# Kernel optimization log

Measured on AMD Instinct MI355X. Metric: run time of the kernel, lower is better.

## Reference

```python
import jax, jax.numpy as jnp
import numpy as np

B, N, C_IN, C_OUT, BASIS = 8, 128, 64, 64, 15
AVG_NOBJ = 49.0
NEG_SLOPE = 0.01  # torch LeakyReLU default


def eops_2_to_2_sum(x, average_nobj=AVG_NOBJ):
    """x: [B, C, N, N] -> [B, C, 15, N, N].
    5 order-zero ops + 10 sum-aggregation ops (sums normalized by average_nobj,
    double sums by average_nobj**2, as in PELICAN's 'sum' aggregation)."""
    n = x.shape[-1]
    eye = jnp.eye(n, dtype=x.dtype)                       # [N, N]
    d = jnp.diagonal(x, axis1=-2, axis2=-1)               # [B, C, N]
    rowsum = x.sum(-1) / average_nobj                      # [B, C, N]
    colsum = x.sum(-2) / average_nobj                      # [B, C, N]
    trace = d.sum(-1) / average_nobj                       # [B, C]
    allsum = x.sum((-2, -1)) / (average_nobj ** 2)         # [B, C]
    bc = lambda v: jnp.broadcast_to(v, x.shape)
    ops = [
        # --- order zero (no aggregation) ---
        d[..., :, None] * eye,                 # diag(A) embedded on diagonal
        bc(d[..., :, None]),                   # A_ii broadcast along j
        bc(d[..., None, :]),                   # A_jj broadcast along i
        x,                                     # identity
        jnp.swapaxes(x, -1, -2),               # transpose
        # --- aggregation ops ---
        rowsum[..., :, None] * eye,            # row sums on diagonal
        colsum[..., :, None] * eye,            # col sums on diagonal
        trace[..., None, None] * eye,          # trace on diagonal
        allsum[..., None, None] * eye,         # total sum on diagonal
        bc(rowsum[..., :, None]),              # rowsum_i broadcast along j
        bc(rowsum[..., None, :]),              # rowsum_j broadcast along i
        bc(colsum[..., :, None]),              # colsum_i broadcast along j
        bc(colsum[..., None, :]),              # colsum_j broadcast along i
        bc(trace[..., None, None]),            # trace broadcast everywhere
        bc(allsum[..., None, None]),           # total sum broadcast everywhere
    ]
    return jnp.stack(ops, axis=2)              # [B, C, 15, N, N]


def setup_inputs() -> dict:
    key = jax.random.key(0)
    ks = jax.random.split(key, 5)
    inputs = jax.random.normal(ks[0], (B, N, N, C_IN), jnp.float32)
    mask = jnp.ones((B, N, N, 1), jnp.float32)
    nobj = jnp.full((B,), float(N), jnp.float32)
    s_b = float(np.sqrt(1.0 / BASIS))
    s_d = float(np.sqrt(1.0 / C_IN))
    coefs00 = jax.random.normal(ks[1], (C_IN, BASIS), jnp.float32) * s_b
    coefs01 = jax.random.normal(ks[2], (C_OUT, BASIS), jnp.float32) * s_b
    coefs10 = jax.random.normal(ks[3], (C_IN, C_OUT), jnp.float32) * s_d
    coefs11 = jax.random.normal(ks[4], (C_IN, C_OUT), jnp.float32) * s_d
    bias = jnp.zeros((C_OUT,), jnp.float32)
    diag_bias = jnp.zeros((C_OUT,), jnp.float32)
    return {"inputs": inputs, "mask": mask, "nobj": nobj,
            "coefs00": coefs00, "coefs01": coefs01,
            "coefs10": coefs10, "coefs11": coefs11,
            "bias": bias, "diag_bias": diag_bias}


def reference(inputs, mask, nobj, coefs00, coefs01, coefs10, coefs11, bias, diag_bias):
    # inputs: [B, N, N, C_in] -> channels-first for basis construction
    x = jnp.transpose(inputs, (0, 3, 1, 2))                     # [B, C, N, N]
    ops = eops_2_to_2_sum(x)                                    # [B, C, 15, N, N]
    # low-rank reconstructed coefficient tensor [C_in, C_out, 15]
    coefs = (coefs00[:, None, :] * coefs10[:, :, None]
             + coefs01[None, :, :] * coefs11[:, :, None])
    out = jnp.einsum('dsb,ndbij->nijs', coefs, ops)             # [B, N, N, C_out]
    eye = jnp.eye(inputs.shape[1], dtype=out.dtype)[None, :, :, None]
    out = out + bias[None, None, None, :] + eye * diag_bias[None, None, None, :]
    out = jax.nn.leaky_relu(out, NEG_SLOPE)
    return out * mask
```

## Files before the change

### kernel.cpp

```cpp
#include <hip/hip_runtime.h>

#define BB 8
#define NN 128
#define CC 64
#define NT 16
static constexpr float INV_A = 1.0f / 49.0f;

#define OFF_C    0
#define OFF_CB   61440
#define OFF_RS   65536
#define OFF_CS   131072
#define OFF_DV   196608
#define OFF_U1   263168
#define OFF_U2   328704
#define OFF_DG   394240
#define OFF_XB   459776

typedef __attribute__((ext_vector_type(8))) short v8s;
typedef __attribute__((ext_vector_type(4))) float v4f;

static __device__ inline unsigned pack2bf(float a, float b) {
    union { float f; unsigned u; } ua, ub; ua.f = a; ub.f = b;
    return ((ua.u + 0x8000u) >> 16) | ((ub.u + 0x8000u) & 0xffff0000u);
}
static __device__ inline unsigned short f2bf(float a) {
    union { float f; unsigned u; } ua; ua.f = a;
    return (unsigned short)((ua.u + 0x8000u) >> 16);
}

__global__ void k_pre(const float* __restrict__ in,
                      const float* __restrict__ c00, const float* __restrict__ c01,
                      const float* __restrict__ c10, const float* __restrict__ c11,
                      float* __restrict__ ws) {
    if (blockIdx.x >= 512) {
        int idx = (blockIdx.x - 512) * 256 + threadIdx.x;
        if (idx < 15 * 4096) {
            int b = idx >> 12; int r = idx & 4095; int d = r >> 6; int s = r & 63;
            ws[OFF_C + idx] = c00[d * 15 + b] * c10[d * 64 + s] + c01[s * 15 + b] * c11[d * 64 + s];
        } else if (idx < 15 * 4096 + 8192) {
            int k = idx - 15 * 4096;
            int which = k >> 12;
            int r = k & 4095; int s = r >> 6; int d = r & 63;
            int b = 3 + which;
            float v = c00[d * 15 + b] * c10[d * 64 + s] + c01[s * 15 + b] * c11[d * 64 + s];
            unsigned short* cb = (unsigned short*)(ws + OFF_CB);
            cb[s * 128 + which * 64 + d] = f2bf(v);
        }
        return;
    }
    __shared__ float4 part[4][4][16];
    int mode = blockIdx.x >> 8;
    int bb = blockIdx.x & 255;
    int n = bb >> 5; int g0 = (bb & 31) * 4;
    int t = threadIdx.x;
    int q = t >> 6; int ii = (t >> 4) & 3; int d4 = t & 15;
    float4 acc = make_float4(0.f, 0.f, 0.f, 0.f);
    if (mode == 0) {
        int i = g0 + ii;
        float4 dvv = acc; bool hd = false;
        const float* base = in + ((size_t)(n * NN + i)) * NN * CC + d4 * 4;
        unsigned short* xB = (unsigned short*)(ws + OFF_XB)
                           + ((size_t)(n * NN + i)) * NN * CC + d4 * 4;
        for (int j = q * 32; j < q * 32 + 32; ++j) {
            float4 v = *(const float4*)(base + (size_t)j * CC);
            acc.x += v.x; acc.y += v.y; acc.z += v.z; acc.w += v.w;
            uint2 pk; pk.x = pack2bf(v.x, v.y); pk.y = pack2bf(v.z, v.w);
            *(uint2*)(xB + (size_t)j * CC) = pk;
            if (j == i) { dvv = v; hd = true; }
        }
        if (hd) *(float4*)(ws + OFF_DV + ((size_t)(n * NN + i)) * CC + d4 * 4) = dvv;
    } else {
        int j = g0 + ii;
        for (int i = q * 32; i < q * 32 + 32; ++i) {
            float4 v = *(const float4*)(in + (((size_t)(n * NN + i)) * NN + j) * CC + d4 * 4);
            acc.x += v.x; acc.y += v.y; acc.z += v.z; acc.w += v.w;
        }
    }
    part[q][ii][d4] = acc;
    __syncthreads();
    if (t < 64) {
        int i2 = t >> 4; int dd = t & 15;
        float4 a = part[0][i2][dd], b = part[1][i2][dd], c = part[2][i2][dd], d = part[3][i2][dd];
        float4 s;
        s.x = (a.x + b.x + c.x + d.x) * INV_A;
        s.y = (a.y + b.y + c.y + d.y) * INV_A;
        s.z = (a.z + b.z + c.z + d.z) * INV_A;
        s.w = (a.w + b.w + c.w + d.w) * INV_A;
        *(float4*)(ws + (mode ? OFF_CS : OFF_RS) + ((size_t)(n * NN + g0 + i2)) * CC + dd * 4) = s;
    }
}

__global__ __launch_bounds__(256, 4) void k_uv(const float* __restrict__ bias,
                                               const float* __restrict__ dbias,
                                               float* __restrict__ ws) {
    __shared__ float trL[64], asL[64];
    __shared__ float pU1[4][4][64], pU2[4][4][64], pDG[4][4][64];
    __shared__ float pS[4][64], pDGc[4][64];
    int n = blockIdx.x >> 5; int i0 = (blockIdx.x & 31) * 4;
    int t = threadIdx.x;
    int s = t & 63; int q = t >> 6;

    {
        float tr = 0.f, as = 0.f;
        #pragma unroll 4
        for (int e = 0; e < 32; ++e) {
            int i = q * 32 + e;
            tr += ws[OFF_DV + ((size_t)(n * NN + i)) * CC + s];
            as += ws[OFF_RS + ((size_t)(n * NN + i)) * CC + s];
        }
        pS[q][s] = tr; pDGc[q][s] = as;
        __syncthreads();
        if (t < 64) {
            trL[t] = (pS[0][t] + pS[1][t] + pS[2][t] + pS[3][t]) * INV_A;
            asL[t] = (pDGc[0][t] + pDGc[1][t] + pDGc[2][t] + pDGc[3][t]) * INV_A;
        }
        __syncthreads();
    }

    const float* C = ws + OFF_C;
    float aU1[4] = {0, 0, 0, 0}, aU2[4] = {0, 0, 0, 0}, aDG[4] = {0, 0, 0, 0};
    float aS = 0.f, aDGc = 0.f;
    #pragma unroll
    for (int c4 = 0; c4 < 4; ++c4) {
        int dc = q * 4 + c4;
        float tr4[4], as4[4], dv4[4][4], rs4[4][4], cs4[4][4];
        #pragma unroll
        for (int k = 0; k < 4; ++k) { tr4[k] = trL[dc * 4 + k]; as4[k] = asL[dc * 4 + k]; }
        #pragma unroll
        for (int ii = 0; ii < 4; ++ii) {
            size_t ro = ((size_t)(n * NN + i0 + ii)) * CC + dc * 4;
            float4 v = *(const float4*)(ws + OFF_DV + ro);
            dv4[ii][0] = v.x; dv4[ii][1] = v.y; dv4[ii][2] = v.z; dv4[ii][3] = v.w;
            float4 r = *(const float4*)(ws + OFF_RS + ro);
            rs4[ii][0] = r.x; rs4[ii][1] = r.y; rs4[ii][2] = r.z; rs4[ii][3] = r.w;
            float4 c = *(const float4*)(ws + OFF_CS + ro);
            cs4[ii][0] = c.x; cs4[ii][1] = c.y; cs4[ii][2] = c.z; cs4[ii][3] = c.w;
        }
        #pragma unroll
        for (int k = 0; k < 4; ++k) {
            int d = dc * 4 + k;
            const float* Cd = C + d * 64 + s;
            float c0 = Cd[0 * 4096], c1 = Cd[1 * 4096], c2 = Cd[2 * 4096];
            float c5 = Cd[5 * 4096], c6 = Cd[6 * 4096], c7 = Cd[7 * 4096];
            float c8 = Cd[8 * 4096], c9 = Cd[9 * 4096], c10v = Cd[10 * 4096];
            float c11v = Cd[11 * 4096], c12v = Cd[12 * 4096];
            float c13 = Cd[13 * 4096], c14 = Cd[14 * 4096];
            aS += c13 * tr4[k] + c14 * as4[k];
            aDGc += c7 * tr4[k] + c8 * as4[k];
            #pragma unroll
            for (int ii = 0; ii < 4; ++ii) {
                aU1[ii] += c1 * dv4[ii][k] + c9 * rs4[ii][k] + c11v * cs4[ii][k];
                aU2[ii] += c2 * dv4[ii][k] + c10v * rs4[ii][k] + c12v * cs4[ii][k];
                aDG[ii] += c0 * dv4[ii][k] + c5 * rs4[ii][k] + c6 * cs4[ii][k];
            }
        }
    }
    #pragma unroll
    for (int ii = 0; ii < 4; ++ii) {
        pU1[q][ii][s] = aU1[ii]; pU2[q][ii][s] = aU2[ii]; pDG[q][ii][s] = aDG[ii];
    }
    pS[q][s] = aS; pDGc[q][s] = aDGc;
    __syncthreads();

    int fi = q;
    float u1 = pU1[0][fi][s] + pU1[1][fi][s] + pU1[2][fi][s] + pU1[3][fi][s];
    float u2 = pU2[0][fi][s] + pU2[1][fi][s] + pU2[2][fi][s] + pU2[3][fi][s];
    float dg = pDG[0][fi][s] + pDG[1][fi][s] + pDG[2][fi][s] + pDG[3][fi][s];
    float aSt = pS[0][s] + pS[1][s] + pS[2][s] + pS[3][s];
    float aDGct = pDGc[0][s] + pDGc[1][s] + pDGc[2][s] + pDGc[3][s];
    size_t row = ((size_t)(n * NN + i0 + fi)) * CC + s;
    ws[OFF_U1 + row] = u1 + aSt + bias[s];
    ws[OFF_U2 + row] = u2;
    ws[OFF_DG + row] = dg + aDGct + dbias[s];
}

__global__ __launch_bounds__(256, 4) void k_main(
        const float* __restrict__ mask,
        const float* __restrict__ ws, float* __restrict__ out) {
    __shared__ __align__(16) unsigned char smem[34816];
    unsigned short* Ab = (unsigned short*)smem;
    unsigned short* Bb = (unsigned short*)(smem + 17408);
    float* Obuf = (float*)smem;

    int blk = blockIdx.x;
    int n = blk / 136; int rem = blk - n * 136;
    int I = 0;
    { int rr = rem; while (rr >= NT - I) { rr -= NT - I; ++I; } rem = rr; }
    int J = I + rem;
    int i0 = I * 8, j0 = J * 8;
    int t = threadIdx.x;
    int tp = t >> 4; int c = t & 15;

    const unsigned short* cb = (const unsigned short*)(ws + OFF_CB);
    #pragma unroll
    for (int e = 0; e < 4; ++e) {
        int s = e * 16 + tp;
        float4 v = *(const float4*)(cb + s * 128 + c * 8);
        *(float4*)((unsigned char*)(Bb + s * 136 + c * 8)) = v;
    }
    const unsigned short* xb = (const unsigned short*)(ws + OFF_XB);
    #pragma unroll
    for (int e = 0; e < 4; ++e) {
        int idx = e * 256 + t;
        int chunk = idx & 7; int row = idx >> 3;
        int hh = row >> 6; int p = row & 63;
        int ii = p >> 3, jj = p & 7;
        int gi = hh ? (j0 + jj) : (i0 + ii);
        int gj = hh ? (i0 + ii) : (j0 + jj);
        float4 v = *(const float4*)(xb + (((size_t)(n * NN + gi)) * NN + gj) * CC + chunk * 8);
        *(float4*)((unsigned char*)(Ab + p * 136 + hh * 64 + chunk * 8)) = v;
    }
    __syncthreads();

    int w = t >> 6; int l = t & 63;
    int r16 = l & 15; int quad = l >> 4;
    int arow = w * 16 + r16;
    v8s af[4];
    #pragma unroll
    for (int kk = 0; kk < 4; ++kk)
        af[kk] = *(const v8s*)(Ab + arow * 136 + kk * 32 + quad * 8);
    v4f acc1[4], acc2[4];
    #pragma unroll
    for (int st = 0; st < 4; ++st) { acc1[st] = 0.f; acc2[st] = 0.f; }
    #pragma unroll
    for (int kk = 0; kk < 4; ++kk) {
        #pragma unroll
        for (int st = 0; st < 4; ++st) {
            v8s bfr = *(const v8s*)(Bb + (st * 16 + r16) * 136 + kk * 32 + quad * 8);
            acc1[st] = __builtin_amdgcn_mfma_f32_16x16x32_bf16(af[kk], bfr, acc1[st], 0, 0, 0);
            acc2[st] = __builtin_amdgcn_mfma_f32_16x16x32_bf16(af[(kk + 2) & 3], bfr, acc2[st], 0, 0, 0);
        }
    }

    #pragma unroll
    for (int st = 0; st < 4; ++st)
        #pragma unroll
        for (int reg = 0; reg < 4; ++reg)
            Obuf[(w * 16 + quad * 4 + reg) * 68 + st * 16 + r16] = acc1[st][reg];
    __syncthreads();
    #pragma unroll
    for (int e = 0; e < 4; ++e) {
        int p = e * 16 + tp;
        int gi = i0 + (p >> 3), gj = j0 + (p & 7);
        size_t prow = ((size_t)(n * NN + gi));
        float4 v = *(const float4*)(Obuf + p * 68 + c * 4);
        float4 u1 = *(const float4*)(ws + OFF_U1 + prow * CC + c * 4);
        float4 u2 = *(const float4*)(ws + OFF_U2 + ((size_t)(n * NN + gj)) * CC + c * 4);
        v.x += u1.x + u2.x; v.y += u1.y + u2.y; v.z += u1.z + u2.z; v.w += u1.w + u2.w;
        if (gi == gj) {
            float4 dg = *(const float4*)(ws + OFF_DG + prow * CC + c * 4);
            v.x += dg.x; v.y += dg.y; v.z += dg.z; v.w += dg.w;
        }
        v.x = v.x > 0.f ? v.x : 0.01f * v.x;
        v.y = v.y > 0.f ? v.y : 0.01f * v.y;
        v.z = v.z > 0.f ? v.z : 0.01f * v.z;
        v.w = v.w > 0.f ? v.w : 0.01f * v.w;
        float m = mask[prow * NN + gj];
        v.x *= m; v.y *= m; v.z *= m; v.w *= m;
        *(float4*)(out + (prow * NN + gj) * CC + c * 4) = v;
    }

    if (I == J) return;
    __syncthreads();
    #pragma unroll
    for (int st = 0; st < 4; ++st)
        #pragma unroll
        for (int reg = 0; reg < 4; ++reg)
            Obuf[(w * 16 + quad * 4 + reg) * 68 + st * 16 + r16] = acc2[st][reg];
    __syncthreads();
    #pragma unroll
    for (int e = 0; e < 4; ++e) {
        int p = e * 16 + tp;
        int gi = j0 + (p & 7), gj = i0 + (p >> 3);
        size_t prow = ((size_t)(n * NN + gi));
        float4 v = *(const float4*)(Obuf + p * 68 + c * 4);
        float4 u1 = *(const float4*)(ws + OFF_U1 + prow * CC + c * 4);
        float4 u2 = *(const float4*)(ws + OFF_U2 + ((size_t)(n * NN + gj)) * CC + c * 4);
        v.x += u1.x + u2.x; v.y += u1.y + u2.y; v.z += u1.z + u2.z; v.w += u1.w + u2.w;
        v.x = v.x > 0.f ? v.x : 0.01f * v.x;
        v.y = v.y > 0.f ? v.y : 0.01f * v.y;
        v.z = v.z > 0.f ? v.z : 0.01f * v.z;
        v.w = v.w > 0.f ? v.w : 0.01f * v.w;
        float m = mask[prow * NN + gj];
        v.x *= m; v.y *= m; v.z *= m; v.w *= m;
        *(float4*)(out + (prow * NN + gj) * CC + c * 4) = v;
    }
}

extern "C" void kernel_launch(void* const* d_in, const int* in_sizes, int n_in,
                              void* d_out, int out_size, void* d_ws, size_t ws_size,
                              hipStream_t stream) {
    const float* inputs = (const float*)d_in[0];
    const float* mask   = (const float*)d_in[1];
    const float* c00 = (const float*)d_in[3];
    const float* c01 = (const float*)d_in[4];
    const float* c10 = (const float*)d_in[5];
    const float* c11 = (const float*)d_in[6];
    const float* bias  = (const float*)d_in[7];
    const float* dbias = (const float*)d_in[8];
    float* out = (float*)d_out;
    float* ws = (float*)d_ws;

    k_pre <<<784, 256, 0, stream>>>(inputs, c00, c01, c10, c11, ws);
    k_uv  <<<256, 256, 0, stream>>>(bias, dbias, ws);
    k_main<<<8 * 136, 256, 0, stream>>>(mask, ws, out);
}
```

Measured before the change: 139.0 us.

## Fuse k_uv into k_main, computing row/col vectors via bf16 MFMA per tile

Drops the separate k_uv kernel. Each k_main block now stages bf16 copies of the DV/RS/CS rows it needs into shared memory and computes the U1/U2 row/column terms with extra MFMA calls against bf16 coefficient slices that k_pre prepares. The trace and allsum reductions and the diagonal term are recomputed per block. This saves one kernel launch and the global round trip for U1/U2/DG, at the cost of redundant per-block work (every block reduces all 128 rows for the trace), lower bf16 precision for the U terms, and more shared memory with occupancy dropped to 3.

```diff
diff --git a/kernel.cpp b/kernel.cpp
--- a/kernel.cpp
+++ b/kernel.cpp
@@ -8,13 +8,12 @@
 
 #define OFF_C    0
 #define OFF_CB   61440
-#define OFF_RS   65536
-#define OFF_CS   131072
-#define OFF_DV   196608
-#define OFF_U1   263168
-#define OFF_U2   328704
-#define OFF_DG   394240
-#define OFF_XB   459776
+#define OFF_CU1  65536
+#define OFF_CU2  71680
+#define OFF_RS   77824
+#define OFF_CS   143360
+#define OFF_DV   208896
+#define OFF_XB   274432
 
 typedef __attribute__((ext_vector_type(8))) short v8s;
 typedef __attribute__((ext_vector_type(4))) float v4f;
@@ -26,6 +25,9 @@
 static __device__ inline unsigned short f2bf(float a) {
     union { float f; unsigned u; } ua; ua.f = a;
     return (unsigned short)((ua.u + 0x8000u) >> 16);
+}
+static __device__ inline float bf2f(unsigned short h) {
+    union { unsigned u; float f; } c; c.u = ((unsigned)h) << 16; return c.f;
 }
 
 __global__ void k_pre(const float* __restrict__ in,
@@ -34,17 +36,28 @@
                       float* __restrict__ ws) {
     if (blockIdx.x >= 512) {
         int idx = (blockIdx.x - 512) * 256 + threadIdx.x;
-        if (idx < 15 * 4096) {
+        if (idx < 61440) {
             int b = idx >> 12; int r = idx & 4095; int d = r >> 6; int s = r & 63;
             ws[OFF_C + idx] = c00[d * 15 + b] * c10[d * 64 + s] + c01[s * 15 + b] * c11[d * 64 + s];
-        } else if (idx < 15 * 4096 + 8192) {
-            int k = idx - 15 * 4096;
+        } else if (idx < 69632) {
+            int k = idx - 61440;
             int which = k >> 12;
             int r = k & 4095; int s = r >> 6; int d = r & 63;
             int b = 3 + which;
             float v = c00[d * 15 + b] * c10[d * 64 + s] + c01[s * 15 + b] * c11[d * 64 + s];
             unsigned short* cb = (unsigned short*)(ws + OFF_CB);
             cb[s * 128 + which * 64 + d] = f2bf(v);
+        } else {
+            int e = idx - 69632;
+            int which = e >= 12288;
+            int r = which ? e - 12288 : e;
+            int s = r / 192; int k = r - s * 192;
+            int f = k >> 6; int d = k & 63;
+            const int b1[3] = {1, 9, 11}, b2[3] = {2, 10, 12};
+            int b = which ? b2[f] : b1[f];
+            float v = c00[d * 15 + b] * c10[d * 64 + s] + c01[s * 15 + b] * c11[d * 64 + s];
+            unsigned short* cu = (unsigned short*)(ws + (which ? OFF_CU2 : OFF_CU1));
+            cu[s * 192 + k] = f2bf(v);
         }
         return;
     }
@@ -90,97 +103,21 @@
     }
 }
 
-__global__ __launch_bounds__(256, 4) void k_uv(const float* __restrict__ bias,
-                                               const float* __restrict__ dbias,
-                                               float* __restrict__ ws) {
-    __shared__ float trL[64], asL[64];
-    __shared__ float pU1[4][4][64], pU2[4][4][64], pDG[4][4][64];
-    __shared__ float pS[4][64], pDGc[4][64];
-    int n = blockIdx.x >> 5; int i0 = (blockIdx.x & 31) * 4;
-    int t = threadIdx.x;
-    int s = t & 63; int q = t >> 6;
-
-    {
-        float tr = 0.f, as = 0.f;
-        #pragma unroll 4
-        for (int e = 0; e < 32; ++e) {
-            int i = q * 32 + e;
-            tr += ws[OFF_DV + ((size_t)(n * NN + i)) * CC + s];
-            as += ws[OFF_RS + ((size_t)(n * NN + i)) * CC + s];
-        }
-        pS[q][s] = tr; pDGc[q][s] = as;
-        __syncthreads();
-        if (t < 64) {
-            trL[t] = (pS[0][t] + pS[1][t] + pS[2][t] + pS[3][t]) * INV_A;
-            asL[t] = (pDGc[0][t] + pDGc[1][t] + pDGc[2][t] + pDGc[3][t]) * INV_A;
-        }
-        __syncthreads();
-    }
-
-    const float* C = ws + OFF_C;
-    float aU1[4] = {0, 0, 0, 0}, aU2[4] = {0, 0, 0, 0}, aDG[4] = {0, 0, 0, 0};
-    float aS = 0.f, aDGc = 0.f;
-    #pragma unroll
-    for (int c4 = 0; c4 < 4; ++c4) {
-        int dc = q * 4 + c4;
-        float tr4[4], as4[4], dv4[4][4], rs4[4][4], cs4[4][4];
-        #pragma unroll
-        for (int k = 0; k < 4; ++k) { tr4[k] = trL[dc * 4 + k]; as4[k] = asL[dc * 4 + k]; }
-        #pragma unroll
-        for (int ii = 0; ii < 4; ++ii) {
-            size_t ro = ((size_t)(n * NN + i0 + ii)) * CC + dc * 4;
-            float4 v = *(const float4*)(ws + OFF_DV + ro);
-            dv4[ii][0] = v.x; dv4[ii][1] = v.y; dv4[ii][2] = v.z; dv4[ii][3] = v.w;
-            float4 r = *(const float4*)(ws + OFF_RS + ro);
-            rs4[ii][0] = r.x; rs4[ii][1] = r.y; rs4[ii][2] = r.z; rs4[ii][3] = r.w;
-            float4 c = *(const float4*)(ws + OFF_CS + ro);
-            cs4[ii][0] = c.x; cs4[ii][1] = c.y; cs4[ii][2] = c.z; cs4[ii][3] = c.w;
-        }
-        #pragma unroll
-        for (int k = 0; k < 4; ++k) {
-            int d = dc * 4 + k;
-            const float* Cd = C + d * 64 + s;
-            float c0 = Cd[0 * 4096], c1 = Cd[1 * 4096], c2 = Cd[2 * 4096];
-            float c5 = Cd[5 * 4096], c6 = Cd[6 * 4096], c7 = Cd[7 * 4096];
-            float c8 = Cd[8 * 4096], c9 = Cd[9 * 4096], c10v = Cd[10 * 4096];
-            float c11v = Cd[11 * 4096], c12v = Cd[12 * 4096];
-            float c13 = Cd[13 * 4096], c14 = Cd[14 * 4096];
-            aS += c13 * tr4[k] + c14 * as4[k];
-            aDGc += c7 * tr4[k] + c8 * as4[k];
-            #pragma unroll
-            for (int ii = 0; ii < 4; ++ii) {
-                aU1[ii] += c1 * dv4[ii][k] + c9 * rs4[ii][k] + c11v * cs4[ii][k];
-                aU2[ii] += c2 * dv4[ii][k] + c10v * rs4[ii][k] + c12v * cs4[ii][k];
-                aDG[ii] += c0 * dv4[ii][k] + c5 * rs4[ii][k] + c6 * cs4[ii][k];
-            }
-        }
-    }
-    #pragma unroll
-    for (int ii = 0; ii < 4; ++ii) {
-        pU1[q][ii][s] = aU1[ii]; pU2[q][ii][s] = aU2[ii]; pDG[q][ii][s] = aDG[ii];
-    }
-    pS[q][s] = aS; pDGc[q][s] = aDGc;
-    __syncthreads();
-
-    int fi = q;
-    float u1 = pU1[0][fi][s] + pU1[1][fi][s] + pU1[2][fi][s] + pU1[3][fi][s];
-    float u2 = pU2[0][fi][s] + pU2[1][fi][s] + pU2[2][fi][s] + pU2[3][fi][s];
-    float dg = pDG[0][fi][s] + pDG[1][fi][s] + pDG[2][fi][s] + pDG[3][fi][s];
-    float aSt = pS[0][s] + pS[1][s] + pS[2][s] + pS[3][s];
-    float aDGct = pDGc[0][s] + pDGc[1][s] + pDGc[2][s] + pDGc[3][s];
-    size_t row = ((size_t)(n * NN + i0 + fi)) * CC + s;
-    ws[OFF_U1 + row] = u1 + aSt + bias[s];
-    ws[OFF_U2 + row] = u2;
-    ws[OFF_DG + row] = dg + aDGct + dbias[s];
-}
-
-__global__ __launch_bounds__(256, 4) void k_main(
-        const float* __restrict__ mask,
+__global__ __launch_bounds__(256, 3) void k_main(
+        const float* __restrict__ mask, const float* __restrict__ bias,
+        const float* __restrict__ dbias,
         const float* __restrict__ ws, float* __restrict__ out) {
-    __shared__ __align__(16) unsigned char smem[34816];
-    unsigned short* Ab = (unsigned short*)smem;
-    unsigned short* Bb = (unsigned short*)(smem + 17408);
+    __shared__ __align__(16) unsigned char smem[52608];
+    unsigned short* Ab  = (unsigned short*)smem;
+    unsigned short* Bb  = (unsigned short*)(smem + 17408);
+    unsigned short* RVb = (unsigned short*)(smem + 34816);
+    float* U1L = (float*)(smem + 41216);
+    float* U2L = (float*)(smem + 45568);
+    float* dgL = (float*)(smem + 49920);
+    float* trL = (float*)(smem + 52096);
+    float* asL = (float*)(smem + 52352);
     float* Obuf = (float*)smem;
+    float* trP  = U1L;
 
     int blk = blockIdx.x;
     int n = blk / 136; int rem = blk - n * 136;
@@ -210,6 +147,42 @@
         float4 v = *(const float4*)(xb + (((size_t)(n * NN + gi)) * NN + gj) * CC + chunk * 8);
         *(float4*)((unsigned char*)(Ab + p * 136 + hh * 64 + chunk * 8)) = v;
     }
+    #pragma unroll
+    for (int r2 = 0; r2 < 2; ++r2) {
+        int ci = t + r2 * 256;
+        if (ci < 384) {
+            int row = ci / 24; int remc = ci - row * 24;
+            int f = remc >> 3; int ch = remc & 7;
+            int grow = row < 8 ? (i0 + row) : (j0 + row - 8);
+            int foff = (f == 0) ? OFF_DV : (f == 1 ? OFF_RS : OFF_CS);
+            const float* src = ws + foff + ((size_t)(n * NN + grow)) * CC + ch * 8;
+            float4 a = *(const float4*)(src);
+            float4 b = *(const float4*)(src + 4);
+            uint4 pk;
+            pk.x = pack2bf(a.x, a.y); pk.y = pack2bf(a.z, a.w);
+            pk.z = pack2bf(b.x, b.y); pk.w = pack2bf(b.z, b.w);
+            *(uint4*)((unsigned char*)(RVb + row * 200 + f * 64 + ch * 8)) = pk;
+        }
+    }
+    int q = t >> 6; int s0 = t & 63;
+    {
+        float pd = 0.f, pr = 0.f;
+        #pragma unroll 4
+        for (int e = 0; e < 32; ++e) {
+            int i = q * 32 + e;
+            pd += ws[OFF_DV + ((size_t)(n * NN + i)) * CC + s0];
+            pr += ws[OFF_RS + ((size_t)(n * NN + i)) * CC + s0];
+        }
+        trP[q * 64 + s0] = pd;
+        trP[(4 + q) * 64 + s0] = pr;
+    }
+    __syncthreads();
+    if (t < 128) {
+        int h = t >> 6; int ss = t & 63;
+        const float* p = trP + h * 256;
+        float v = p[ss] + p[64 + ss] + p[128 + ss] + p[192 + ss];
+        (h ? asL : trL)[ss] = v * INV_A;
+    }
     __syncthreads();
 
     int w = t >> 6; int l = t & 63;
@@ -231,24 +204,87 @@
             acc2[st] = __builtin_amdgcn_mfma_f32_16x16x32_bf16(af[(kk + 2) & 3], bfr, acc2[st], 0, 0, 0);
         }
     }
+    v4f aU1 = 0.f, aU2 = 0.f;
+    {
+        const unsigned short* cu1 = (const unsigned short*)(ws + OFF_CU1);
+        const unsigned short* cu2 = (const unsigned short*)(ws + OFF_CU2);
+        int sg = w * 16 + r16;
+        #pragma unroll
+        for (int kk = 0; kk < 6; ++kk) {
+            v8s a1 = *(const v8s*)(cu1 + sg * 192 + kk * 32 + quad * 8);
+            v8s a2 = *(const v8s*)(cu2 + sg * 192 + kk * 32 + quad * 8);
+            v8s bv = *(const v8s*)(RVb + r16 * 200 + kk * 32 + quad * 8);
+            aU1 = __builtin_amdgcn_mfma_f32_16x16x32_bf16(a1, bv, aU1, 0, 0, 0);
+            aU2 = __builtin_amdgcn_mfma_f32_16x16x32_bf16(a2, bv, aU2, 0, 0, 0);
+        }
+    }
+    float sS[4] = {0.f, 0.f, 0.f, 0.f};
+    {
+        const float* C13 = ws + OFF_C + 13 * 4096;
+        const float* C14 = ws + OFF_C + 14 * 4096;
+        for (int d = 0; d < 64; ++d) {
+            float4 a = *(const float4*)(C13 + d * 64 + c * 4);
+            float4 b = *(const float4*)(C14 + d * 64 + c * 4);
+            float tv = trL[d], av = asL[d];
+            sS[0] += tv * a.x + av * b.x;
+            sS[1] += tv * a.y + av * b.y;
+            sS[2] += tv * a.z + av * b.z;
+            sS[3] += tv * a.w + av * b.w;
+        }
+    }
+    if (I == J) {
+        const float* Cb0 = ws + OFF_C;
+        float dg0 = 0.f, dg1 = 0.f, dgc = 0.f;
+        int rg = t >> 6;
+        for (int d = 0; d < 64; ++d) {
+            float c0v = Cb0[0 * 4096 + d * 64 + s0];
+            float c5v = Cb0[5 * 4096 + d * 64 + s0];
+            float c6v = Cb0[6 * 4096 + d * 64 + s0];
+            float c7v = Cb0[7 * 4096 + d * 64 + s0];
+            float c8v = Cb0[8 * 4096 + d * 64 + s0];
+            float dva = bf2f(RVb[rg * 200 + d]);
+            float rsa = bf2f(RVb[rg * 200 + 64 + d]);
+            float csa = bf2f(RVb[rg * 200 + 128 + d]);
+            float dvb = bf2f(RVb[(rg + 4) * 200 + d]);
+            float rsb = bf2f(RVb[(rg + 4) * 200 + 64 + d]);
+            float csb = bf2f(RVb[(rg + 4) * 200 + 128 + d]);
+            dg0 += c0v * dva + c5v * rsa + c6v * csa;
+            dg1 += c0v * dvb + c5v * rsb + c6v * csb;
+            dgc += c7v * trL[d] + c8v * asL[d];
+        }
+        float db = dbias[s0];
+        dgL[rg * 68 + s0] = dg0 + dgc + db;
+        dgL[(rg + 4) * 68 + s0] = dg1 + dgc + db;
+    }
 
     #pragma unroll
     for (int st = 0; st < 4; ++st)
         #pragma unroll
         for (int reg = 0; reg < 4; ++reg)
             Obuf[(w * 16 + quad * 4 + reg) * 68 + st * 16 + r16] = acc1[st][reg];
-    __syncthreads();
+    #pragma unroll
+    for (int reg = 0; reg < 4; ++reg) {
+        U1L[r16 * 68 + w * 16 + quad * 4 + reg] = aU1[reg];
+        U2L[r16 * 68 + w * 16 + quad * 4 + reg] = aU2[reg];
+    }
+    __syncthreads();
+
+    float4 bias4 = *(const float4*)(bias + c * 4);
     #pragma unroll
     for (int e = 0; e < 4; ++e) {
         int p = e * 16 + tp;
-        int gi = i0 + (p >> 3), gj = j0 + (p & 7);
+        int ii = p >> 3, jj = p & 7;
+        int gi = i0 + ii, gj = j0 + jj;
         size_t prow = ((size_t)(n * NN + gi));
         float4 v = *(const float4*)(Obuf + p * 68 + c * 4);
-        float4 u1 = *(const float4*)(ws + OFF_U1 + prow * CC + c * 4);
-        float4 u2 = *(const float4*)(ws + OFF_U2 + ((size_t)(n * NN + gj)) * CC + c * 4);
-        v.x += u1.x + u2.x; v.y += u1.y + u2.y; v.z += u1.z + u2.z; v.w += u1.w + u2.w;
+        float4 u1 = *(const float4*)(U1L + ii * 68 + c * 4);
+        float4 u2 = *(const float4*)(U2L + (8 + jj) * 68 + c * 4);
+        v.x += u1.x + u2.x + sS[0] + bias4.x;
+        v.y += u1.y + u2.y + sS[1] + bias4.y;
+        v.z += u1.z + u2.z + sS[2] + bias4.z;
+        v.w += u1.w + u2.w + sS[3] + bias4.w;
         if (gi == gj) {
-            float4 dg = *(const float4*)(ws + OFF_DG + prow * CC + c * 4);
+            float4 dg = *(const float4*)(dgL + ii * 68 + c * 4);
             v.x += dg.x; v.y += dg.y; v.z += dg.z; v.w += dg.w;
         }
         v.x = v.x > 0.f ? v.x : 0.01f * v.x;
@@ -271,12 +307,16 @@
     #pragma unroll
     for (int e = 0; e < 4; ++e) {
         int p = e * 16 + tp;
-        int gi = j0 + (p & 7), gj = i0 + (p >> 3);
+        int ii = p >> 3, jj = p & 7;
+        int gi = j0 + jj, gj = i0 + ii;
         size_t prow = ((size_t)(n * NN + gi));
         float4 v = *(const float4*)(Obuf + p * 68 + c * 4);
-        float4 u1 = *(const float4*)(ws + OFF_U1 + prow * CC + c * 4);
-        float4 u2 = *(const float4*)(ws + OFF_U2 + ((size_t)(n * NN + gj)) * CC + c * 4);
-        v.x += u1.x + u2.x; v.y += u1.y + u2.y; v.z += u1.z + u2.z; v.w += u1.w + u2.w;
+        float4 u1 = *(const float4*)(U1L + (8 + jj) * 68 + c * 4);
+        float4 u2 = *(const float4*)(U2L + ii * 68 + c * 4);
+        v.x += u1.x + u2.x + sS[0] + bias4.x;
+        v.y += u1.y + u2.y + sS[1] + bias4.y;
+        v.z += u1.z + u2.z + sS[2] + bias4.z;
+        v.w += u1.w + u2.w + sS[3] + bias4.w;
         v.x = v.x > 0.f ? v.x : 0.01f * v.x;
         v.y = v.y > 0.f ? v.y : 0.01f * v.y;
         v.z = v.z > 0.f ? v.z : 0.01f * v.z;
@@ -301,7 +341,6 @@
     float* out = (float*)d_out;
     float* ws = (float*)d_ws;
 
-    k_pre <<<784, 256, 0, stream>>>(inputs, c00, c01, c10, c11, ws);
-    k_uv  <<<256, 256, 0, stream>>>(bias, dbias, ws);
-    k_main<<<8 * 136, 256, 0, stream>>>(mask, ws, out);
-}
+    k_pre <<<880, 256, 0, stream>>>(inputs, c00, c01, c10, c11, ws);
+    k_main<<<8 * 136, 256, 0, stream>>>(mask, bias, dbias, ws, out);
+}
```

Result: slower. 164.0 us (+18.0%).
